# Kernel optimization log

Hardware: AMD Instinct MI355X
Metric: run time of the kernel (lower is better)

The kernel has to match this reference:

```python
import jax, jax.numpy as jnp
import numpy as np

B, N = 1, 512
NODE_DIM, EDGE_DIM = 384, 128
H, SK, SV, PK, PV = 8, 16, 16, 4, 4
EPS = 1e-8
LN_EPS = 1e-5


def setup_inputs() -> dict:
    key = jax.random.key(0)
    ks = jax.random.split(key, 20)
    d, e = NODE_DIM, EDGE_DIM
    s = 0.02
    rn = lambda k, sh: jax.random.normal(k, sh, jnp.float32) * s
    # orthonormal per-residue rotations (valid rigid frames)
    R, _ = jnp.linalg.qr(jax.random.normal(ks[2], (B, N, 3, 3), jnp.float32))
    out_dim = H * (SV + EDGE_DIM + PV * 4)  # scalar + pairwise + points(3) + point norms(1)
    return dict(
        node_features=jax.random.normal(ks[0], (B, N, d), jnp.float32),
        edge_features=jax.random.normal(ks[1], (B, N, N, e), jnp.float32),
        rotations=R,
        translations=jax.random.normal(ks[3], (B, N, 3), jnp.float32),
        mask=jnp.ones((B, N), bool),
        Wq_s=rn(ks[4], (d, H * SK)), Wk_s=rn(ks[5], (d, H * SK)), Wv_s=rn(ks[6], (d, H * SV)),
        Wq_p=rn(ks[7], (d, H * PK * 3)), Wk_p=rn(ks[8], (d, H * PK * 3)), Wv_p=rn(ks[9], (d, H * PV * 3)),
        point_weights=jnp.full((H,), np.log(np.e - 1.0), jnp.float32),  # softplus -> 1
        Wb=rn(ks[10], (e, H)), bb=jnp.zeros((H,), jnp.float32),
        Wo=rn(ks[11], (out_dim, d)), bo=jnp.zeros((d,), jnp.float32),
        g1=jnp.ones((d,), jnp.float32), beta1=jnp.zeros((d,), jnp.float32),
        W1=rn(ks[12], (d, 2 * d)), b1=jnp.zeros((2 * d,), jnp.float32),
        W2=rn(ks[13], (2 * d, 2 * d)), b2=jnp.zeros((2 * d,), jnp.float32),
        W3=rn(ks[14], (2 * d, d)), b3=jnp.zeros((d,), jnp.float32),
        g2=jnp.ones((d,), jnp.float32), beta2=jnp.zeros((d,), jnp.float32),
    )


def _layer_norm(x, g, b):
    mu = x.mean(-1, keepdims=True)
    var = ((x - mu) ** 2).mean(-1, keepdims=True)
    return (x - mu) * jax.lax.rsqrt(var + LN_EPS) * g + b


def _forward(node_features, edge_features, rotations, translations, mask,
             Wq_s, Wk_s, Wv_s, Wq_p, Wk_p, Wv_p, point_weights, Wb, bb, Wo, bo,
             g1, beta1, W1, b1, W2, b2, W3, b3, g2, beta2):
    b, n, d = node_features.shape
    # num_attn_logits = 3 (scalar + point + pairwise)
    scal_scale = (3 * SK) ** -0.5
    point_scale = (3 * PK * 4.5) ** -0.5
    pair_scale = 3 ** -0.5

    qs = (node_features @ Wq_s).reshape(b, n, H, SK)
    kk = (node_features @ Wk_s).reshape(b, n, H, SK)
    vs = (node_features @ Wv_s).reshape(b, n, H, SV)

    def apply_rigid(p):  # p: (b,n,h,d,3); global = R^T applied per lucidrains einsum + t
        return jnp.einsum('bnhdc,bncr->bnhdr', p, rotations) + translations[:, :, None, None, :]

    qp = apply_rigid((node_features @ Wq_p).reshape(b, n, H, PK, 3))
    kp = apply_rigid((node_features @ Wk_p).reshape(b, n, H, PK, 3))
    vp = apply_rigid((node_features @ Wv_p).reshape(b, n, H, PV, 3))

    logits = jnp.einsum('bihk,bjhk->bhij', qs, kk) * scal_scale

    # point distance term: sum_{d,c} (q-k)^2 = |q|^2 + |k|^2 - 2 q.k (avoids (b,h,i,j,d,3) tensor)
    w = jax.nn.softplus(point_weights)  # (H,)
    q2 = jnp.einsum('bnhdc,bnhdc->bhn', qp, qp)
    k2 = jnp.einsum('bnhdc,bnhdc->bhn', kp, kp)
    cross = jnp.einsum('bihdc,bjhdc->bhij', qp, kp)
    dist = q2[..., :, None] + k2[..., None, :] - 2.0 * cross  # (b,h,i,j)
    logits = logits - 0.5 * point_scale * w[None, :, None, None] * dist

    pair_bias = (jnp.einsum('bije,eh->bhij', edge_features, Wb) + bb[None, :, None, None]) * pair_scale
    logits = logits + pair_bias

    pm = mask[:, None, :, None] & mask[:, None, None, :]  # (b,1,i,j)
    logits = jnp.where(pm, logits, -jnp.finfo(logits.dtype).max)
    attn = jax.nn.softmax(logits, axis=-1)  # (b,h,i,j)

    rs = jnp.einsum('bhij,bjhv->bihv', attn, vs).reshape(b, n, H * SV)
    rp = jnp.einsum('bhij,bije->bihe', attn, edge_features).reshape(b, n, H * EDGE_DIM)
    pts = jnp.einsum('bhij,bjhdc->bihdc', attn, vp)
    # invert rigid: subtract t, apply R (inverse of R^T application)
    local = jnp.einsum('bihdc,birc->bihdr', pts - translations[:, :, None, None, :], rotations)
    norms = jnp.sqrt((local ** 2).sum(-1) + EPS)  # (b,n,H,PV)

    cat = jnp.concatenate([rs, local.reshape(b, n, H * PV * 3), norms.reshape(b, n, H * PV), rp], axis=-1)
    ipa_out = cat @ Wo + bo

    x = _layer_norm(ipa_out, g1, beta1)  # dropout is identity at eval
    x = jax.nn.relu(x @ W1 + b1)
    x = jax.nn.relu(x @ W2 + b2)
    x = x @ W3 + b3
    return _layer_norm(x, g2, beta2)


def reference(node_features, edge_features, rotations, translations, mask,
              Wq_s, Wk_s, Wv_s, Wq_p, Wk_p, Wv_p, point_weights, Wb, bb, Wo, bo,
              g1, beta1, W1, b1, W2, b2, W3, b3, g2, beta2):
    return _forward(node_features, edge_features, rotations, translations, mask,
                    Wq_s, Wk_s, Wv_s, Wq_p, Wk_p, Wv_p, point_weights, Wb, bb, Wo, bo,
                    g1, beta1, W1, b1, W2, b2, W3, b3, g2, beta2)
```

## Files before the change

### kernel.cpp

```cpp
#include <hip/hip_runtime.h>
#include <cstddef>

#define NN 512
#define DD 384
#define EE 128
#define HH 8
#define JSPLIT 16

static constexpr float SCAL_SCALE  = 0.1443375673f;
static constexpr float POINT_SCALE = 0.1360827635f;
static constexpr float PAIR_SCALE  = 0.5773502692f;
static constexpr float LN_EPS = 1e-5f;
static constexpr float EPS    = 1e-8f;

typedef __bf16 bf16x8 __attribute__((ext_vector_type(8)));
typedef float  f32x4  __attribute__((ext_vector_type(4)));

__device__ __forceinline__ unsigned short bf16_bits(float v) {
    union { __bf16 b; unsigned short s; } c; c.b = (__bf16)v; return c.s;
}
__device__ __forceinline__ float bits2f(unsigned u) {
    union { unsigned u; float f; } c; c.u = u; return c.f;
}

__global__ __launch_bounds__(256) void prep_weights_kernel(
    const float* __restrict__ Wo, const float* __restrict__ W1,
    const float* __restrict__ W2, const float* __restrict__ W3,
    const float* __restrict__ Wq_s, const float* __restrict__ Wk_s,
    const float* __restrict__ Wv_s,
    const float* __restrict__ Wq_p, const float* __restrict__ Wk_p,
    const float* __restrict__ Wv_p, const float* __restrict__ nf,
    unsigned short* __restrict__ WoT, unsigned short* __restrict__ W1T,
    unsigned short* __restrict__ W2T, unsigned short* __restrict__ W3T,
    unsigned short* __restrict__ WprojT, unsigned short* __restrict__ nfb)
{
    const int b = blockIdx.x;
    if (b >= 1884) {
        const int idx = (b - 1884) * 1024 + threadIdx.x * 4;
        float4 v = *(const float4*)(nf + idx);
        unsigned lo = bf16_bits(v.x) | ((unsigned)bf16_bits(v.y) << 16);
        unsigned hi = bf16_bits(v.z) | ((unsigned)bf16_bits(v.w) << 16);
        uint2 pk; pk.x = lo; pk.y = hi;
        *(uint2*)(nfb + idx) = pk;
        return;
    }
    const float* W; unsigned short* out;
    int K, N, tile, rowoff = 0;
    if (b < 480)       { W = Wo;   out = WoT;    K = 1280; N = 384; tile = b; }
    else if (b < 768)  { W = W1;   out = W1T;    K = 384;  N = 768; tile = b - 480; }
    else if (b < 1344) { W = W2;   out = W2T;    K = 768;  N = 768; tile = b - 768; }
    else if (b < 1632) { W = W3;   out = W3T;    K = 768;  N = 384; tile = b - 1344; }
    else if (b < 1680) { W = Wq_s; out = WprojT; K = 384;  N = 128; tile = b - 1632; rowoff = 0; }
    else if (b < 1728) { W = Wk_s; out = WprojT; K = 384;  N = 128; tile = b - 1680; rowoff = 128; }
    else if (b < 1776) { W = Wv_s; out = WprojT; K = 384;  N = 128; tile = b - 1728; rowoff = 256; }
    else if (b < 1812) { W = Wq_p; out = WprojT; K = 384;  N = 96;  tile = b - 1776; rowoff = 384; }
    else if (b < 1848) { W = Wk_p; out = WprojT; K = 384;  N = 96;  tile = b - 1812; rowoff = 480; }
    else               { W = Wv_p; out = WprojT; K = 384;  N = 96;  tile = b - 1848; rowoff = 576; }

    const int ntn = N / 32;
    const int n0 = (tile % ntn) * 32, k0 = (tile / ntn) * 32;
    __shared__ float tb[32][33];
    const int tx = threadIdx.x & 31, ty = threadIdx.x >> 5;
    #pragma unroll
    for (int dy = 0; dy < 32; dy += 8)
        tb[ty + dy][tx] = W[(size_t)(k0 + ty + dy) * N + n0 + tx];
    __syncthreads();
    #pragma unroll
    for (int dy = 0; dy < 32; dy += 8)
        out[(size_t)(rowoff + n0 + ty + dy) * K + k0 + tx] = bf16_bits(tb[tx][ty + dy]);
}

template <int K, int NOUT, bool RELU, bool HASB, bool OUTBF>
__global__ __launch_bounds__(256) void gemm_bf16(
    const unsigned short* __restrict__ Xb, const unsigned short* __restrict__ Wt,
    const float* __restrict__ bias, void* __restrict__ Yv)
{
    const int t = threadIdx.x;
    const int w = t >> 6, lane = t & 63;
    const int r = lane & 15, q = lane >> 4;
    const int n0 = blockIdx.x * 16;
    const int m0 = blockIdx.y * 64 + w * 16;

    const unsigned short* xrow = Xb + (size_t)(m0 + r) * K + q * 8;
    const unsigned short* wrow = Wt + (size_t)(n0 + r) * K + q * 8;

    f32x4 acc = {0.f, 0.f, 0.f, 0.f};
    #pragma unroll 4
    for (int k0 = 0; k0 < K; k0 += 32) {
        union { uint4 u; bf16x8 v; } au, bu;
        au.u = *(const uint4*)(xrow + k0);
        bu.u = *(const uint4*)(wrow + k0);
        acc = __builtin_amdgcn_mfma_f32_16x16x32_bf16(au.v, bu.v, acc, 0, 0, 0);
    }
    const int n = n0 + r;
    const float bi = HASB ? bias[n] : 0.f;
    #pragma unroll
    for (int reg = 0; reg < 4; reg++) {
        const int m = m0 + q * 4 + reg;
        float v = acc[reg] + bi;
        if (RELU) v = fmaxf(v, 0.f);
        if (OUTBF) ((unsigned short*)Yv)[(size_t)m * NOUT + n] = bf16_bits(v);
        else       ((float*)Yv)[(size_t)m * NOUT + n] = v;
    }
}

__global__ __launch_bounds__(256) void ipa_post_kernel(
    const float* __restrict__ proj_out, const float* __restrict__ rot,
    const float* __restrict__ trans, const float* __restrict__ pw,
    const float* __restrict__ bb,
    unsigned short* __restrict__ Qp, unsigned short* __restrict__ Kp,
    unsigned short* __restrict__ svT)
{
    const int i = blockIdx.x;
    const int t = threadIdx.x;
    __shared__ float outs[672];
    __shared__ float ptg[288];
    __shared__ float q2s[8], k2s[8], pwh[8];

    for (int f = t; f < 672; f += 256) outs[f] = proj_out[(size_t)i * 672 + f];
    if (t < 8) pwh[t] = 0.5f * POINT_SCALE * log1pf(expf(pw[t]));
    __syncthreads();

    for (int f = t; f < 288; f += 256) {
        int which = f / 96, idx = f % 96;
        int hd = idx / 3, r = idx % 3;
        float acc = trans[(size_t)i * 3 + r];
        #pragma unroll
        for (int c = 0; c < 3; c++)
            acc += outs[384 + which * 96 + hd * 3 + c] * rot[(size_t)i * 9 + c * 3 + r];
        ptg[f] = acc;
    }
    __syncthreads();
    if (t < 16) {
        int which = t / 8, h = t % 8;
        float acc = 0.f;
        #pragma unroll
        for (int m = 0; m < 12; m++) {
            float v = ptg[which * 96 + h * 12 + m];
            acc += v * v;
        }
        (which ? k2s : q2s)[h] = acc;
    }
    __syncthreads();

    {
        const int h = t >> 5, d = t & 31;
        float qv, kv;
        if (d < 16)      { qv = outs[h * 16 + d] * SCAL_SCALE; kv = outs[128 + h * 16 + d]; }
        else if (d < 28) { qv = ptg[h * 12 + d - 16] * (2.f * pwh[h]); kv = ptg[96 + h * 12 + d - 16]; }
        else if (d == 28){ qv = -pwh[h] * q2s[h]; kv = 1.f; }
        else if (d == 29){ qv = 1.f; kv = -pwh[h] * k2s[h]; }
        else if (d == 30){ qv = 1.f; kv = bb[h] * PAIR_SCALE; }
        else             { qv = 0.f; kv = 0.f; }
        Qp[((size_t)i * 8 + h) * 32 + d] = bf16_bits(qv);
        Kp[((size_t)i * 8 + h) * 32 + d] = bf16_bits(kv);
    }
    if (t < 128) {
        int h = t >> 4, v = t & 15;
        svT[((size_t)h * 32 + v) * NN + i] = bf16_bits(outs[256 + h * 16 + v]);
    } else if (t < 224) {
        int idx = t - 128, h = idx / 12, m = idx % 12;
        svT[((size_t)h * 32 + 16 + m) * NN + i] = bf16_bits(ptg[192 + idx]);
    } else {
        int idx = t - 224;
        int h = idx >> 2, m = 28 + (idx & 3);
        svT[((size_t)h * 32 + m) * NN + i] = 0;
    }
}

__global__ __launch_bounds__(256) void ipa_fused2(
    const float* __restrict__ edge,
    const unsigned short* __restrict__ Qp, const unsigned short* __restrict__ Kp,
    const unsigned short* __restrict__ svT, const float* __restrict__ Wb,
    float* __restrict__ Opart, float* __restrict__ Mpart, float* __restrict__ Lpart)
{
    const int js = blockIdx.x;
    const int it = blockIdx.y;
    const int i0 = it * 8;
    const int jbase = js * 32;
    const int t = threadIdx.x;
    const int w = t >> 6, lane = t & 63;
    const int r = lane & 15, q = lane >> 4;

    __shared__ float Lqk[64 * 33];
    __shared__ __align__(16) unsigned short P1[72 * 32];
    __shared__ __align__(16) unsigned short P2[72 * 32];
    __shared__ __align__(16) unsigned short wbTl[16 * 136];
    __shared__ __align__(16) unsigned short eT[4 * 128 * 40];

    if (t < 128) {
        float4 a = *(const float4*)&Wb[t * 8];
        float4 b = *(const float4*)&Wb[t * 8 + 4];
        wbTl[0 * 136 + t] = bf16_bits(a.x * PAIR_SCALE);
        wbTl[1 * 136 + t] = bf16_bits(a.y * PAIR_SCALE);
        wbTl[2 * 136 + t] = bf16_bits(a.z * PAIR_SCALE);
        wbTl[3 * 136 + t] = bf16_bits(a.w * PAIR_SCALE);
        wbTl[4 * 136 + t] = bf16_bits(b.x * PAIR_SCALE);
        wbTl[5 * 136 + t] = bf16_bits(b.y * PAIR_SCALE);
        wbTl[6 * 136 + t] = bf16_bits(b.z * PAIR_SCALE);
        wbTl[7 * 136 + t] = bf16_bits(b.w * PAIR_SCALE);
    }

    #pragma unroll
    for (int hh = 0; hh < 2; hh++) {
        const int h = w * 2 + hh;
        bf16x8 aq = *(const bf16x8*)&Qp[((size_t)(i0 + (r & 7)) * 8 + h) * 32 + q * 8];
        #pragma unroll
        for (int jt = 0; jt < 2; jt++) {
            bf16x8 bk = *(const bf16x8*)&Kp[((size_t)(jbase + jt * 16 + r) * 8 + h) * 32 + q * 8];
            f32x4 acc = {0.f, 0.f, 0.f, 0.f};
            acc = __builtin_amdgcn_mfma_f32_16x16x32_bf16(aq, bk, acc, 0, 0, 0);
            if (q < 2) {
                #pragma unroll
                for (int reg = 0; reg < 4; reg++)
                    Lqk[(h * 8 + q * 4 + reg) * 33 + jt * 16 + r] = acc[reg];
            }
        }
    }
    __syncthreads();

    const int te = t >> 1, th8 = t & 1;

    for (int half = 0; half < 2; half++) {
        #pragma unroll
        for (int k = 0; k < 4; k++) {
            const int i = i0 + half * 4 + k;
            const float* src = edge + ((size_t)i * 512 + jbase + th8 * 16) * 128 + te;
            float v[16];
            #pragma unroll
            for (int s = 0; s < 16; s++) v[s] = src[(size_t)s * 128];
            union { uint4 u2[2]; unsigned short sh[16]; } pk;
            #pragma unroll
            for (int s = 0; s < 16; s++) pk.sh[s] = bf16_bits(v[s]);
            unsigned short* dst = &eT[k * 5120 + te * 40 + th8 * 16];
            *(uint4*)(dst + 0) = pk.u2[0];
            *(uint4*)(dst + 8) = pk.u2[1];
        }
        {
            const int il = half * 4 + w;
            const float* ebase = edge + ((size_t)(i0 + il) * 512 + jbase) * 128;
            #pragma unroll
            for (int jt = 0; jt < 2; jt++) {
                f32x4 acc = {0.f, 0.f, 0.f, 0.f};
                #pragma unroll
                for (int kk = 0; kk < 4; kk++) {
                    const float* srcb = ebase + (size_t)(jt * 16 + r) * 128 + kk * 32 + q * 8;
                    float4 f0 = *(const float4*)srcb;
                    float4 f1 = *(const float4*)(srcb + 4);
                    union { uint4 u; bf16x8 v; } aE;
                    aE.u.x = (unsigned)bf16_bits(f0.x) | ((unsigned)bf16_bits(f0.y) << 16);
                    aE.u.y = (unsigned)bf16_bits(f0.z) | ((unsigned)bf16_bits(f0.w) << 16);
                    aE.u.z = (unsigned)bf16_bits(f1.x) | ((unsigned)bf16_bits(f1.y) << 16);
                    aE.u.w = (unsigned)bf16_bits(f1.z) | ((unsigned)bf16_bits(f1.w) << 16);
                    union { uint4 u; bf16x8 v; } bW;
                    bW.u = *(const uint4*)&wbTl[r * 136 + kk * 32 + q * 8];
                    acc = __builtin_amdgcn_mfma_f32_16x16x32_bf16(aE.v, bW.v, acc, 0, 0, 0);
                }
                if (r < 8) {
                    #pragma unroll
                    for (int reg = 0; reg < 4; reg++)
                        Lqk[(r * 8 + il) * 33 + jt * 16 + q * 4 + reg] += acc[reg];
                }
            }
        }
        __syncthreads();

        if (t < 32) {
            const int h = t >> 2, il = half * 4 + (t & 3);
            const float* lrow = &Lqk[(h * 8 + il) * 33];
            float lg[32];
            float mx = -1e30f;
            #pragma unroll
            for (int j = 0; j < 32; j++) {
                lg[j] = lrow[j];
                mx = fmaxf(mx, lg[j]);
            }
            float sum = 0.f;
            #pragma unroll
            for (int j = 0; j < 32; j++) { lg[j] = __expf(lg[j] - mx); sum += lg[j]; }
            Mpart[(size_t)(js * 64 + it) * 64 + h * 8 + il] = mx;
            Lpart[(size_t)(js * 64 + it) * 64 + h * 8 + il] = sum;
            unsigned pk[16];
            #pragma unroll
            for (int s = 0; s < 16; s++)
                pk[s] = (unsigned)bf16_bits(lg[2 * s]) | ((unsigned)bf16_bits(lg[2 * s + 1]) << 16);
            uint4* d1 = (uint4*)&P1[((size_t)il * 8 + h) * 32];
            uint4* d2 = (uint4*)&P2[((size_t)h * 8 + il) * 32];
            #pragma unroll
            for (int s = 0; s < 4; s++) {
                uint4 v; v.x = pk[4*s]; v.y = pk[4*s+1]; v.z = pk[4*s+2]; v.w = pk[4*s+3];
                d1[s] = v; d2[s] = v;
            }
        }
        __syncthreads();

        {
            const int il = half * 4 + w;
            union { uint4 u; bf16x8 v; } bP;
            bP.u = *(const uint4*)&P1[((size_t)il * 8 + r) * 32 + q * 8];
            union { uint4 u; bf16x8 v; } aF[8];
            #pragma unroll
            for (int eb = 0; eb < 8; eb++)
                aF[eb].u = *(const uint4*)&eT[w * 5120 + (eb * 16 + r) * 40 + q * 8];
            f32x4 acc[8];
            #pragma unroll
            for (int eb = 0; eb < 8; eb++) {
                f32x4 c = {0.f, 0.f, 0.f, 0.f};
                acc[eb] = __builtin_amdgcn_mfma_f32_16x16x32_bf16(aF[eb].v, bP.v, c, 0, 0, 0);
            }
            float* orw = Opart + (size_t)((js * 64 + it) * 8 + il) * 1248;
            if (r < 8) {
                #pragma unroll
                for (int eb = 0; eb < 8; eb++)
                    *(f32x4*)&orw[r * 156 + 28 + eb * 16 + q * 4] = acc[eb];
            }
        }
        __syncthreads();
    }

    #pragma unroll
    for (int hh = 0; hh < 2; hh++) {
        const int h = w * 2 + hh;
        union { uint4 u; bf16x8 v; } aP;
        aP.u = *(const uint4*)&P2[((size_t)h * 8 + r) * 32 + q * 8];
        #pragma unroll
        for (int ct = 0; ct < 2; ct++) {
            union { uint4 u; bf16x8 v; } bS;
            bS.u = *(const uint4*)&svT[((size_t)h * 32 + ct * 16 + r) * 512 + jbase + q * 8];
            f32x4 c = {0.f, 0.f, 0.f, 0.f};
            f32x4 acc = __builtin_amdgcn_mfma_f32_16x16x32_bf16(aP.v, bS.v, c, 0, 0, 0);
            const int cc = ct * 16 + r;
            if (q < 2 && cc < 28) {
                #pragma unroll
                for (int reg = 0; reg < 4; reg++) {
                    const int i = q * 4 + reg;
                    Opart[((size_t)((js * 64 + it) * 8 + i)) * 1248 + h * 156 + cc] = acc[reg];
                }
            }
        }
    }
}

__global__ __launch_bounds__(256) void ipa_merge(
    const float* __restrict__ Opart, const float* __restrict__ Mpart,
    const float* __restrict__ Lpart, const float* __restrict__ rot,
    const float* __restrict__ trans, unsigned short* __restrict__ cat_bf)
{
    const int i = blockIdx.x;
    const int itile = i >> 3, il = i & 7;
    const int t = threadIdx.x;
    __shared__ float wn[8 * JSPLIT];
    __shared__ float pts_s[96];

    if (t < 8) {
        const int h = t;
        float ms[JSPLIT], ls[JSPLIT], M = -1e30f;
        #pragma unroll
        for (int s = 0; s < JSPLIT; s++) {
            ms[s] = Mpart[(size_t)(s * 64 + itile) * 64 + h * 8 + il];
            ls[s] = Lpart[(size_t)(s * 64 + itile) * 64 + h * 8 + il];
            M = fmaxf(M, ms[s]);
        }
        float denom = 0.f, e[JSPLIT];
        #pragma unroll
        for (int s = 0; s < JSPLIT; s++) { e[s] = __expf(ms[s] - M); denom += e[s] * ls[s]; }
        const float inv = 1.f / denom;
        #pragma unroll
        for (int s = 0; s < JSPLIT; s++) wn[h * JSPLIT + s] = e[s] * inv;
    }
    __syncthreads();

    for (int col = t; col < 1248; col += 256) {
        const int h = col / 156, c = col % 156;
        float acc = 0.f;
        #pragma unroll
        for (int s = 0; s < JSPLIT; s++)
            acc += wn[h * JSPLIT + s] *
                   Opart[((size_t)(s * 64 + itile) * 8 + il) * 1248 + col];
        if (c < 16)      cat_bf[(size_t)i * 1280 + h * 16 + c] = bf16_bits(acc);
        else if (c < 28) pts_s[h * 12 + (c - 16)] = acc;
        else             cat_bf[(size_t)i * 1280 + 256 + h * 128 + (c - 28)] = bf16_bits(acc);
    }
    __syncthreads();

    const float* tr = trans + (size_t)i * 3;
    const float* R  = rot + (size_t)i * 9;
    if (t < 96) {
        int hd = t / 3, rr = t % 3;
        float acc = 0.f;
        #pragma unroll
        for (int c = 0; c < 3; c++)
            acc += (pts_s[hd * 3 + c] - tr[c]) * R[rr * 3 + c];
        cat_bf[(size_t)i * 1280 + 128 + t] = bf16_bits(acc);
    } else if (t < 128) {
        int pv = t - 96;
        float s = EPS;
        #pragma unroll
        for (int rr = 0; rr < 3; rr++) {
            float v = 0.f;
            #pragma unroll
            for (int c = 0; c < 3; c++)
                v += (pts_s[pv * 3 + c] - tr[c]) * R[rr * 3 + c];
            s += v * v;
        }
        cat_bf[(size_t)i * 1280 + 224 + pv] = bf16_bits(sqrtf(s));
    }
}

template <bool OUTBF>
__global__ __launch_bounds__(256) void ln_kernel(
    const float* __restrict__ X, const float* __restrict__ g,
    const float* __restrict__ beta, void* __restrict__ Yv, int Dim)
{
    __shared__ float red[4];
    __shared__ float bc;
    const int i = blockIdx.x;
    const int t = threadIdx.x;
    const float* x = X + (size_t)i * Dim;

    float s = 0.f;
    for (int k = t; k < Dim; k += 256) s += x[k];
    #pragma unroll
    for (int off = 32; off; off >>= 1) s += __shfl_down(s, off, 64);
    if ((t & 63) == 0) red[t >> 6] = s;
    __syncthreads();
    if (t == 0) bc = red[0] + red[1] + red[2] + red[3];
    __syncthreads();
    const float mu = bc / Dim;

    float v = 0.f;
    for (int k = t; k < Dim; k += 256) { float d = x[k] - mu; v += d * d; }
    #pragma unroll
    for (int off = 32; off; off >>= 1) v += __shfl_down(v, off, 64);
    __syncthreads();
    if ((t & 63) == 0) red[t >> 6] = v;
    __syncthreads();
    if (t == 0) bc = red[0] + red[1] + red[2] + red[3];
    __syncthreads();
    const float rstd = rsqrtf(bc / Dim + LN_EPS);

    for (int k = t; k < Dim; k += 256) {
        float val = (x[k] - mu) * rstd * g[k] + beta[k];
        if (OUTBF) ((unsigned short*)Yv)[(size_t)i * Dim + k] = bf16_bits(val);
        else       ((float*)Yv)[(size_t)i * Dim + k] = val;
    }
}

extern "C" void kernel_launch(void* const* d_in, const int* in_sizes, int n_in,
                              void* d_out, int out_size, void* d_ws, size_t ws_size,
                              hipStream_t stream)
{
    const float* nf    = (const float*)d_in[0];
    const float* edge  = (const float*)d_in[1];
    const float* rot   = (const float*)d_in[2];
    const float* trans = (const float*)d_in[3];
    const float* Wq_s = (const float*)d_in[5];
    const float* Wk_s = (const float*)d_in[6];
    const float* Wv_s = (const float*)d_in[7];
    const float* Wq_p = (const float*)d_in[8];
    const float* Wk_p = (const float*)d_in[9];
    const float* Wv_p = (const float*)d_in[10];
    const float* pw   = (const float*)d_in[11];
    const float* Wb   = (const float*)d_in[12];
    const float* bb   = (const float*)d_in[13];
    const float* Wo   = (const float*)d_in[14];
    const float* bo   = (const float*)d_in[15];
    const float* g1   = (const float*)d_in[16];
    const float* be1  = (const float*)d_in[17];
    const float* W1   = (const float*)d_in[18];
    const float* b1   = (const float*)d_in[19];
    const float* W2   = (const float*)d_in[20];
    const float* b2   = (const float*)d_in[21];
    const float* W3   = (const float*)d_in[22];
    const float* b3   = (const float*)d_in[23];
    const float* g2   = (const float*)d_in[24];
    const float* be2  = (const float*)d_in[25];

    float* ws = (float*)d_ws;
    float* proj_out = ws;
    float* ipa   = proj_out + 344064;
    float* y     = ipa + 196608;
    float* Opart = y + 196608;
    float* Mpart = Opart + 10223616;
    float* Lpart = Mpart + 65536;
    unsigned short* cat_bf = (unsigned short*)(Lpart + 65536);
    unsigned short* x1b = cat_bf + 655360;
    unsigned short* h1b = x1b + 196608;
    unsigned short* h2b = h1b + 393216;
    unsigned short* Qp  = h2b + 393216;
    unsigned short* Kp  = Qp + 131072;
    unsigned short* svT = Kp + 131072;
    unsigned short* WoT = svT + 131072;
    unsigned short* W1T = WoT + 491520;
    unsigned short* W2T = W1T + 294912;
    unsigned short* W3T = W2T + 589824;
    unsigned short* WprojT = W3T + 294912;
    unsigned short* nfb = WprojT + 258048;

    prep_weights_kernel<<<2076, 256, 0, stream>>>(Wo, W1, W2, W3,
                                                  Wq_s, Wk_s, Wv_s, Wq_p, Wk_p, Wv_p, nf,
                                                  WoT, W1T, W2T, W3T, WprojT, nfb);

    gemm_bf16<384, 672, false, false, false><<<dim3(42, 8), 256, 0, stream>>>(nfb, WprojT, nullptr, proj_out);

    ipa_post_kernel<<<NN, 256, 0, stream>>>(proj_out, rot, trans, pw, bb, Qp, Kp, svT);

    ipa_fused2<<<dim3(JSPLIT, 64), 256, 0, stream>>>(edge, Qp, Kp, svT, Wb,
                                                     Opart, Mpart, Lpart);

    ipa_merge<<<NN, 256, 0, stream>>>(Opart, Mpart, Lpart, rot, trans, cat_bf);

    gemm_bf16<1280, 384, false, true, false><<<dim3(24, 8), 256, 0, stream>>>(cat_bf, WoT, bo, ipa);
    ln_kernel<true><<<NN, 256, 0, stream>>>(ipa, g1, be1, x1b, 384);

    gemm_bf16<384, 768, true, true, true><<<dim3(48, 8), 256, 0, stream>>>(x1b, W1T, b1, h1b);
    gemm_bf16<768, 768, true, true, true><<<dim3(48, 8), 256, 0, stream>>>(h1b, W2T, b2, h2b);
    gemm_bf16<768, 384, false, true, false><<<dim3(24, 8), 256, 0, stream>>>(h2b, W3T, b3, y);

    ln_kernel<false><<<NN, 256, 0, stream>>>(y, g2, be2, d_out, 384);
}
```

Baseline: 335.6 us.

## Fuse fp32-to-bf16 conversion and first LayerNorm into GEMM loads, swizzle edge LDS

The separate node-feature bf16 conversion blocks are removed from the weight-prep kernel, and the projection GEMM now reads fp32 input and converts it inline. The first LayerNorm kernel is dropped; the W1 GEMM computes per-row mean and variance itself and normalizes while loading. In the attention kernel, the padded edge-transpose LDS layout is replaced by an XOR swizzle to cut LDS footprint and avoid bank conflicts, and the Wb tile is halved. The cost is redundant LayerNorm statistics computed by every column block, plus a one-pass variance formula.

Measured after the change: 349.3 us. 1.04x slower.

```diff
diff --git a/kernel.cpp b/kernel.cpp
--- a/kernel.cpp
+++ b/kernel.cpp
@@ -29,21 +29,12 @@
     const float* __restrict__ Wq_s, const float* __restrict__ Wk_s,
     const float* __restrict__ Wv_s,
     const float* __restrict__ Wq_p, const float* __restrict__ Wk_p,
-    const float* __restrict__ Wv_p, const float* __restrict__ nf,
+    const float* __restrict__ Wv_p,
     unsigned short* __restrict__ WoT, unsigned short* __restrict__ W1T,
     unsigned short* __restrict__ W2T, unsigned short* __restrict__ W3T,
-    unsigned short* __restrict__ WprojT, unsigned short* __restrict__ nfb)
+    unsigned short* __restrict__ WprojT)
 {
     const int b = blockIdx.x;
-    if (b >= 1884) {
-        const int idx = (b - 1884) * 1024 + threadIdx.x * 4;
-        float4 v = *(const float4*)(nf + idx);
-        unsigned lo = bf16_bits(v.x) | ((unsigned)bf16_bits(v.y) << 16);
-        unsigned hi = bf16_bits(v.z) | ((unsigned)bf16_bits(v.w) << 16);
-        uint2 pk; pk.x = lo; pk.y = hi;
-        *(uint2*)(nfb + idx) = pk;
-        return;
-    }
     const float* W; unsigned short* out;
     int K, N, tile, rowoff = 0;
     if (b < 480)       { W = Wo;   out = WoT;    K = 1280; N = 384; tile = b; }
@@ -70,10 +61,11 @@
         out[(size_t)(rowoff + n0 + ty + dy) * K + k0 + tx] = bf16_bits(tb[tx][ty + dy]);
 }
 
-template <int K, int NOUT, bool RELU, bool HASB, bool OUTBF>
+template <int K, int NOUT, bool RELU, bool HASB, bool OUTBF, int XM>
 __global__ __launch_bounds__(256) void gemm_bf16(
-    const unsigned short* __restrict__ Xb, const unsigned short* __restrict__ Wt,
-    const float* __restrict__ bias, void* __restrict__ Yv)
+    const void* __restrict__ Xv, const unsigned short* __restrict__ Wt,
+    const float* __restrict__ bias, void* __restrict__ Yv,
+    const float* __restrict__ lng, const float* __restrict__ lnb)
 {
     const int t = threadIdx.x;
     const int w = t >> 6, lane = t & 63;
@@ -81,14 +73,57 @@
     const int n0 = blockIdx.x * 16;
     const int m0 = blockIdx.y * 64 + w * 16;
 
-    const unsigned short* xrow = Xb + (size_t)(m0 + r) * K + q * 8;
+    const unsigned short* xrow = nullptr;
+    const float* xrowf = nullptr;
+    if constexpr (XM == 0) xrow = (const unsigned short*)Xv + (size_t)(m0 + r) * K + q * 8;
+    else                   xrowf = (const float*)Xv + (size_t)(m0 + r) * K + q * 8;
     const unsigned short* wrow = Wt + (size_t)(n0 + r) * K + q * 8;
+
+    float mu = 0.f, rstd = 0.f;
+    if constexpr (XM == 2) {
+        float s = 0.f, s2 = 0.f;
+        #pragma unroll
+        for (int k0 = 0; k0 < K; k0 += 32) {
+            float4 a = *(const float4*)(xrowf + k0);
+            float4 b = *(const float4*)(xrowf + k0 + 4);
+            s  += a.x + a.y + a.z + a.w + b.x + b.y + b.z + b.w;
+            s2 += a.x*a.x + a.y*a.y + a.z*a.z + a.w*a.w
+                + b.x*b.x + b.y*b.y + b.z*b.z + b.w*b.w;
+        }
+        s  += __shfl_xor(s, 16, 64);  s  += __shfl_xor(s, 32, 64);
+        s2 += __shfl_xor(s2, 16, 64); s2 += __shfl_xor(s2, 32, 64);
+        mu = s / (float)K;
+        rstd = rsqrtf(fmaxf(s2 / (float)K - mu * mu, 0.f) + LN_EPS);
+    }
 
     f32x4 acc = {0.f, 0.f, 0.f, 0.f};
     #pragma unroll 4
     for (int k0 = 0; k0 < K; k0 += 32) {
         union { uint4 u; bf16x8 v; } au, bu;
-        au.u = *(const uint4*)(xrow + k0);
+        if constexpr (XM == 0) {
+            au.u = *(const uint4*)(xrow + k0);
+        } else {
+            float4 f0 = *(const float4*)(xrowf + k0);
+            float4 f1 = *(const float4*)(xrowf + k0 + 4);
+            if constexpr (XM == 2) {
+                float4 g0 = *(const float4*)(lng + k0 + q * 8);
+                float4 g1 = *(const float4*)(lng + k0 + q * 8 + 4);
+                float4 c0 = *(const float4*)(lnb + k0 + q * 8);
+                float4 c1 = *(const float4*)(lnb + k0 + q * 8 + 4);
+                f0.x = (f0.x - mu) * rstd * g0.x + c0.x;
+                f0.y = (f0.y - mu) * rstd * g0.y + c0.y;
+                f0.z = (f0.z - mu) * rstd * g0.z + c0.z;
+                f0.w = (f0.w - mu) * rstd * g0.w + c0.w;
+                f1.x = (f1.x - mu) * rstd * g1.x + c1.x;
+                f1.y = (f1.y - mu) * rstd * g1.y + c1.y;
+                f1.z = (f1.z - mu) * rstd * g1.z + c1.z;
+                f1.w = (f1.w - mu) * rstd * g1.w + c1.w;
+            }
+            au.v[0] = (__bf16)f0.x; au.v[1] = (__bf16)f0.y;
+            au.v[2] = (__bf16)f0.z; au.v[3] = (__bf16)f0.w;
+            au.v[4] = (__bf16)f1.x; au.v[5] = (__bf16)f1.y;
+            au.v[6] = (__bf16)f1.z; au.v[7] = (__bf16)f1.w;
+        }
         bu.u = *(const uint4*)(wrow + k0);
         acc = __builtin_amdgcn_mfma_f32_16x16x32_bf16(au.v, bu.v, acc, 0, 0, 0);
     }
@@ -185,8 +220,8 @@
     __shared__ float Lqk[64 * 33];
     __shared__ __align__(16) unsigned short P1[72 * 32];
     __shared__ __align__(16) unsigned short P2[72 * 32];
-    __shared__ __align__(16) unsigned short wbTl[16 * 136];
-    __shared__ __align__(16) unsigned short eT[4 * 128 * 40];
+    __shared__ __align__(16) unsigned short wbTl[8 * 136];
+    __shared__ __align__(16) unsigned short eT[4 * 128 * 32];
 
     if (t < 128) {
         float4 a = *(const float4*)&Wb[t * 8];
@@ -232,9 +267,9 @@
             union { uint4 u2[2]; unsigned short sh[16]; } pk;
             #pragma unroll
             for (int s = 0; s < 16; s++) pk.sh[s] = bf16_bits(v[s]);
-            unsigned short* dst = &eT[k * 5120 + te * 40 + th8 * 16];
-            *(uint4*)(dst + 0) = pk.u2[0];
-            *(uint4*)(dst + 8) = pk.u2[1];
+            unsigned short* dst = &eT[k * 4096 + te * 32];
+            *(uint4*)(dst + (((2 * th8)     ^ (te & 3)) * 8)) = pk.u2[0];
+            *(uint4*)(dst + (((2 * th8 + 1) ^ (te & 3)) * 8)) = pk.u2[1];
         }
         {
             const int il = half * 4 + w;
@@ -253,7 +288,7 @@
                     aE.u.z = (unsigned)bf16_bits(f1.x) | ((unsigned)bf16_bits(f1.y) << 16);
                     aE.u.w = (unsigned)bf16_bits(f1.z) | ((unsigned)bf16_bits(f1.w) << 16);
                     union { uint4 u; bf16x8 v; } bW;
-                    bW.u = *(const uint4*)&wbTl[r * 136 + kk * 32 + q * 8];
+                    bW.u = *(const uint4*)&wbTl[(r & 7) * 136 + kk * 32 + q * 8];
                     acc = __builtin_amdgcn_mfma_f32_16x16x32_bf16(aE.v, bW.v, acc, 0, 0, 0);
                 }
                 if (r < 8) {
@@ -301,7 +336,7 @@
             union { uint4 u; bf16x8 v; } aF[8];
             #pragma unroll
             for (int eb = 0; eb < 8; eb++)
-                aF[eb].u = *(const uint4*)&eT[w * 5120 + (eb * 16 + r) * 40 + q * 8];
+                aF[eb].u = *(const uint4*)&eT[w * 4096 + (eb * 16 + r) * 32 + ((q ^ (r & 3)) * 8)];
             f32x4 acc[8];
             #pragma unroll
             for (int eb = 0; eb < 8; eb++) {
@@ -495,13 +530,13 @@
     unsigned short* W2T = W1T + 294912;
     unsigned short* W3T = W2T + 589824;
     unsigned short* WprojT = W3T + 294912;
-    unsigned short* nfb = WprojT + 258048;
-
-    prep_weights_kernel<<<2076, 256, 0, stream>>>(Wo, W1, W2, W3,
-                                                  Wq_s, Wk_s, Wv_s, Wq_p, Wk_p, Wv_p, nf,
-                                                  WoT, W1T, W2T, W3T, WprojT, nfb);
-
-    gemm_bf16<384, 672, false, false, false><<<dim3(42, 8), 256, 0, stream>>>(nfb, WprojT, nullptr, proj_out);
+
+    prep_weights_kernel<<<1884, 256, 0, stream>>>(Wo, W1, W2, W3,
+                                                  Wq_s, Wk_s, Wv_s, Wq_p, Wk_p, Wv_p,
+                                                  WoT, W1T, W2T, W3T, WprojT);
+
+    gemm_bf16<384, 672, false, false, false, 1><<<dim3(42, 8), 256, 0, stream>>>(
+        nf, WprojT, nullptr, proj_out, nullptr, nullptr);
 
     ipa_post_kernel<<<NN, 256, 0, stream>>>(proj_out, rot, trans, pw, bb, Qp, Kp, svT);
 
@@ -510,12 +545,15 @@
 
     ipa_merge<<<NN, 256, 0, stream>>>(Opart, Mpart, Lpart, rot, trans, cat_bf);
 
-    gemm_bf16<1280, 384, false, true, false><<<dim3(24, 8), 256, 0, stream>>>(cat_bf, WoT, bo, ipa);
-    ln_kernel<true><<<NN, 256, 0, stream>>>(ipa, g1, be1, x1b, 384);
-
-    gemm_bf16<384, 768, true, true, true><<<dim3(48, 8), 256, 0, stream>>>(x1b, W1T, b1, h1b);
-    gemm_bf16<768, 768, true, true, true><<<dim3(48, 8), 256, 0, stream>>>(h1b, W2T, b2, h2b);
-    gemm_bf16<768, 384, false, true, false><<<dim3(24, 8), 256, 0, stream>>>(h2b, W3T, b3, y);
+    gemm_bf16<1280, 384, false, true, false, 0><<<dim3(24, 8), 256, 0, stream>>>(
+        cat_bf, WoT, bo, ipa, nullptr, nullptr);
+
+    gemm_bf16<384, 768, true, true, true, 2><<<dim3(48, 8), 256, 0, stream>>>(
+        ipa, W1T, b1, h1b, g1, be1);
+    gemm_bf16<768, 768, true, true, true, 0><<<dim3(48, 8), 256, 0, stream>>>(
+        h1b, W2T, b2, h2b, nullptr, nullptr);
+    gemm_bf16<768, 384, false, true, false, 0><<<dim3(24, 8), 256, 0, stream>>>(
+        h2b, W3T, b3, y, nullptr, nullptr);
 
     ln_kernel<false><<<NN, 256, 0, stream>>>(y, g2, be2, d_out, 384);
 }
```

## Prefetch edge tiles into registers and XOR-swizzle transposed edge LDS buffer

Applied to the files above, without the earlier changes.

Each half's transposed edge loads now go into registers early (before the QK MFMAs, and for the second half right after the first commit). They are converted and written to shared memory only after the pair-bias MFMA, so global latency overlaps other work. The eT buffer drops its 40-element padding for a 32-element stride with an XOR swizzle to avoid bank conflicts, and the unused half of wbTl is removed to cut LDS footprint. It also skips the final barrier of the last half. The cost is 64 extra live floats per thread, which adds register pressure and could reduce occupancy or cause spills.

Measured after the change: 335.2 us. No clear change (-0.1%).

```diff
diff --git a/kernel.cpp b/kernel.cpp
--- a/kernel.cpp
+++ b/kernel.cpp
@@ -185,8 +185,8 @@
     __shared__ float Lqk[64 * 33];
     __shared__ __align__(16) unsigned short P1[72 * 32];
     __shared__ __align__(16) unsigned short P2[72 * 32];
-    __shared__ __align__(16) unsigned short wbTl[16 * 136];
-    __shared__ __align__(16) unsigned short eT[4 * 128 * 40];
+    __shared__ __align__(16) unsigned short wbTl[8 * 136];
+    __shared__ __align__(16) unsigned short eT[4 * 128 * 32];
 
     if (t < 128) {
         float4 a = *(const float4*)&Wb[t * 8];
@@ -201,15 +201,48 @@
         wbTl[7 * 136 + t] = bf16_bits(b.w * PAIR_SCALE);
     }
 
+    const int te = t >> 1, th8 = t & 1;
+    float pf[4][16];
+
+    auto issue_pf = [&](int half) {
+        #pragma unroll
+        for (int k = 0; k < 4; k++) {
+            const float* src = edge + (((size_t)(i0 + half * 4 + k) * 512 + jbase + th8 * 16) * 128) + te;
+            #pragma unroll
+            for (int s = 0; s < 16; s++) pf[k][s] = src[(size_t)s * 128];
+        }
+    };
+    auto commit_pf = [&]() {
+        #pragma unroll
+        for (int k = 0; k < 4; k++) {
+            union { uint4 u2[2]; unsigned short sh[16]; } pk;
+            #pragma unroll
+            for (int s = 0; s < 16; s++) pk.sh[s] = bf16_bits(pf[k][s]);
+            unsigned short* dst = &eT[k * 4096 + te * 32];
+            *(uint4*)(dst + (((2 * th8)     ^ (te & 3)) * 8)) = pk.u2[0];
+            *(uint4*)(dst + (((2 * th8 + 1) ^ (te & 3)) * 8)) = pk.u2[1];
+        }
+    };
+
+    bf16x8 aq[2]; bf16x8 bk[2][2];
     #pragma unroll
     for (int hh = 0; hh < 2; hh++) {
         const int h = w * 2 + hh;
-        bf16x8 aq = *(const bf16x8*)&Qp[((size_t)(i0 + (r & 7)) * 8 + h) * 32 + q * 8];
+        aq[hh] = *(const bf16x8*)&Qp[((size_t)(i0 + (r & 7)) * 8 + h) * 32 + q * 8];
+        #pragma unroll
+        for (int jt = 0; jt < 2; jt++)
+            bk[hh][jt] = *(const bf16x8*)&Kp[((size_t)(jbase + jt * 16 + r) * 8 + h) * 32 + q * 8];
+    }
+
+    issue_pf(0);
+
+    #pragma unroll
+    for (int hh = 0; hh < 2; hh++) {
+        const int h = w * 2 + hh;
         #pragma unroll
         for (int jt = 0; jt < 2; jt++) {
-            bf16x8 bk = *(const bf16x8*)&Kp[((size_t)(jbase + jt * 16 + r) * 8 + h) * 32 + q * 8];
             f32x4 acc = {0.f, 0.f, 0.f, 0.f};
-            acc = __builtin_amdgcn_mfma_f32_16x16x32_bf16(aq, bk, acc, 0, 0, 0);
+            acc = __builtin_amdgcn_mfma_f32_16x16x32_bf16(aq[hh], bk[hh][jt], acc, 0, 0, 0);
             if (q < 2) {
                 #pragma unroll
                 for (int reg = 0; reg < 4; reg++)
@@ -219,23 +252,8 @@
     }
     __syncthreads();
 
-    const int te = t >> 1, th8 = t & 1;
-
+    #pragma unroll
     for (int half = 0; half < 2; half++) {
-        #pragma unroll
-        for (int k = 0; k < 4; k++) {
-            const int i = i0 + half * 4 + k;
-            const float* src = edge + ((size_t)i * 512 + jbase + th8 * 16) * 128 + te;
-            float v[16];
-            #pragma unroll
-            for (int s = 0; s < 16; s++) v[s] = src[(size_t)s * 128];
-            union { uint4 u2[2]; unsigned short sh[16]; } pk;
-            #pragma unroll
-            for (int s = 0; s < 16; s++) pk.sh[s] = bf16_bits(v[s]);
-            unsigned short* dst = &eT[k * 5120 + te * 40 + th8 * 16];
-            *(uint4*)(dst + 0) = pk.u2[0];
-            *(uint4*)(dst + 8) = pk.u2[1];
-        }
         {
             const int il = half * 4 + w;
             const float* ebase = edge + ((size_t)(i0 + il) * 512 + jbase) * 128;
@@ -253,7 +271,7 @@
                     aE.u.z = (unsigned)bf16_bits(f1.x) | ((unsigned)bf16_bits(f1.y) << 16);
                     aE.u.w = (unsigned)bf16_bits(f1.z) | ((unsigned)bf16_bits(f1.w) << 16);
                     union { uint4 u; bf16x8 v; } bW;
-                    bW.u = *(const uint4*)&wbTl[r * 136 + kk * 32 + q * 8];
+                    bW.u = *(const uint4*)&wbTl[(r & 7) * 136 + kk * 32 + q * 8];
                     acc = __builtin_amdgcn_mfma_f32_16x16x32_bf16(aE.v, bW.v, acc, 0, 0, 0);
                 }
                 if (r < 8) {
@@ -263,6 +281,8 @@
                 }
             }
         }
+        commit_pf();
+        if (half == 0) issue_pf(1);
         __syncthreads();
 
         if (t < 32) {
@@ -301,7 +321,7 @@
             union { uint4 u; bf16x8 v; } aF[8];
             #pragma unroll
             for (int eb = 0; eb < 8; eb++)
-                aF[eb].u = *(const uint4*)&eT[w * 5120 + (eb * 16 + r) * 40 + q * 8];
+                aF[eb].u = *(const uint4*)&eT[w * 4096 + (eb * 16 + r) * 32 + ((q ^ (r & 3)) * 8)];
             f32x4 acc[8];
             #pragma unroll
             for (int eb = 0; eb < 8; eb++) {
@@ -315,7 +335,7 @@
                     *(f32x4*)&orw[r * 156 + 28 + eb * 16 + q * 4] = acc[eb];
             }
         }
-        __syncthreads();
+        if (half == 0) __syncthreads();
     }
 
     #pragma unroll
```
